# Kernel tuning notes

Hardware: AMD Instinct MI355X
Metric: run time of the kernel (lower is better)

The kernel has to match this reference:

```python
import jax, jax.numpy as jnp
import numpy as np

N = 20000   # nodes
E = 320000  # edges
F0 = 32     # num_features
H = 8       # GAT heads
G = 64      # graphs in batch


def setup_inputs() -> dict:
    key = jax.random.key(0)
    ks = jax.random.split(key, 16)
    def p(k, shape, s=0.05):
        return jax.random.normal(k, shape, jnp.float32) * s
    d = {}
    d['x'] = jax.random.normal(ks[0], (N, F0), jnp.float32)
    d['edge_index'] = jax.random.randint(ks[1], (2, E), 0, N, dtype=jnp.int32)
    d['edge_weights'] = jax.random.uniform(ks[2], (E,), jnp.float32)
    d['batch'] = jnp.sort(jax.random.randint(ks[3], (N,), 0, G, dtype=jnp.int32))
    # GATConv(32 -> 32, heads=8)
    d['W_gat'] = p(ks[4], (F0, H * F0)); d['att_src'] = p(ks[5], (H, F0))
    d['att_dst'] = p(ks[6], (H, F0));    d['b_gat'] = jnp.zeros((H * F0,), jnp.float32)
    # residual Linear(256 -> 1024) (widened so the residual add is shape-consistent)
    d['W_res'] = p(ks[7], (H * F0, 1024)); d['b_res'] = jnp.zeros((1024,), jnp.float32)
    # GCNConv(256 -> 512) + BN1
    d['W2'] = p(ks[8], (H * F0, 512)); d['b2'] = jnp.zeros((512,), jnp.float32)
    d['g1'] = jnp.ones((512,), jnp.float32); d['be1'] = jnp.zeros((512,), jnp.float32)
    d['m1'] = jnp.zeros((512,), jnp.float32); d['v1'] = jnp.ones((512,), jnp.float32)
    # GCNConv(512 -> 1024) + BN2
    d['W3'] = p(ks[9], (512, 1024)); d['b3'] = jnp.zeros((1024,), jnp.float32)
    d['g2'] = jnp.ones((1024,), jnp.float32); d['be2'] = jnp.zeros((1024,), jnp.float32)
    d['m2'] = jnp.zeros((1024,), jnp.float32); d['v2'] = jnp.ones((1024,), jnp.float32)
    # head
    d['Wf1'] = p(ks[10], (1024, 256)); d['bf1'] = jnp.zeros((256,), jnp.float32)
    d['Wf2'] = p(ks[11], (256, 2));    d['bf2'] = jnp.zeros((2,), jnp.float32)
    return d


def _add_self_loops(edge_index, edge_weight, n):
    loop = jnp.arange(n, dtype=edge_index.dtype)
    ei = jnp.concatenate([edge_index, jnp.stack([loop, loop])], axis=1)
    ew = jnp.concatenate([edge_weight, jnp.ones((n,), edge_weight.dtype)])
    return ei, ew


def _gat(x, edge_index, W, att_src, att_dst, b, n):
    # PyG GATConv, concat=True, eval (attention dropout off). Self-loops already added.
    src, dst = edge_index[0], edge_index[1]
    h = (x @ W).reshape(n, H, -1)                    # [N,H,C]
    a_s = jnp.einsum('nhc,hc->nh', h, att_src)        # [N,H]
    a_d = jnp.einsum('nhc,hc->nh', h, att_dst)
    e = jax.nn.leaky_relu(a_s[src] + a_d[dst], 0.2)   # [E,H]
    m = jax.ops.segment_max(e, dst, num_segments=n)   # softmax over incoming edges
    ex = jnp.exp(e - m[dst])
    s = jax.ops.segment_sum(ex, dst, num_segments=n)
    alpha = ex / s[dst]
    out = jax.ops.segment_sum(h[src] * alpha[:, :, None], dst, num_segments=n)
    return out.reshape(n, -1) + b                     # [N,H*C]


def _gcn(x, edge_index, w, W, b, n):
    # PyG GCNConv with symmetric normalization; self-loops (weight 1) already added.
    src, dst = edge_index[0], edge_index[1]
    deg = jax.ops.segment_sum(w, dst, num_segments=n)
    dinv = jnp.where(deg > 0, jax.lax.rsqrt(jnp.maximum(deg, 1e-12)), 0.0)
    norm = dinv[src] * w * dinv[dst]                  # [E]
    h = x @ W                                         # transform first (cheaper)
    return jax.ops.segment_sum(h[src] * norm[:, None], dst, num_segments=n) + b


def _bn(x, g, b, m, v):
    return g * (x - m) * jax.lax.rsqrt(v + 1e-5) + b


def reference(x, edge_index, edge_weights, batch, W_gat, att_src, att_dst, b_gat,
              W_res, b_res, W2, b2, g1, be1, m1, v1, W3, b3, g2, be2, m2, v2,
              Wf1, bf1, Wf2, bf2):
    n = x.shape[0]
    ei, ew = _add_self_loops(edge_index, edge_weights, n)
    h = jax.nn.relu(_gat(x, ei, W_gat, att_src, att_dst, b_gat, n))   # [N,256]
    res = h @ W_res + b_res                                           # [N,1024]
    h = _gcn(h, ei, ew, W2, b2, n)                                    # [N,512]
    h = jax.nn.relu(_bn(h, g1, be1, m1, v1))
    h = _gcn(h, ei, ew, W3, b3, n)                                    # [N,1024]
    h = jax.nn.relu(_bn(h, g2, be2, m2, v2))
    h = h + res
    pooled = jax.ops.segment_max(h, batch, num_segments=G)            # global max pool [G,1024]
    z = jax.nn.relu(pooled @ Wf1 + bf1)                               # dropout is eval no-op
    return z @ Wf2 + bf2                                              # [G,2]
```

## Files before the change

kernel.cpp:

```cpp
#include <hip/hip_runtime.h>
#include <hip/hip_bf16.h>

#define NN 20000
#define EE 320000
#define GG 64
#define EN (EE + NN)
#define MT 157

typedef float f32x4 __attribute__((ext_vector_type(4)));
typedef __bf16 bf16x4 __attribute__((ext_vector_type(4)));
typedef __bf16 bf16x8 __attribute__((ext_vector_type(8)));

__device__ __forceinline__ void gl_lds16(const void* g, void* l) {
    __builtin_amdgcn_global_load_lds((const __attribute__((address_space(1))) void*)g,
                                     (__attribute__((address_space(3))) void*)l, 16, 0, 0);
}

__global__ void sentinel_kernel(float* out, int n) {
    int i = blockIdx.x * 256 + threadIdx.x;
    if (i < n) out[i] = 12345.0f;
}

__global__ void init_kernel(int* deg_cnt, float* deg_w, int* fill, float* pooled) {
    int i = blockIdx.x * 256 + threadIdx.x;
    if (i < NN) { deg_cnt[i] = 1; deg_w[i] = 1.0f; fill[i] = 0; }
    if (i < GG * 1024) pooled[i] = -INFINITY;
}

__global__ __launch_bounds__(256) void convert_wt(const float* __restrict__ W, __bf16* __restrict__ Wt,
                                                  int K, int N) {
    __shared__ float tile[64][65];
    int kb = blockIdx.y * 64, nb = blockIdx.x * 64;
    int tx = threadIdx.x & 63, ty = threadIdx.x >> 6;
#pragma unroll
    for (int i = ty; i < 64; i += 4)
        tile[i][tx] = W[(size_t)(kb + i) * N + nb + tx];
    __syncthreads();
#pragma unroll
    for (int i = ty; i < 64; i += 4)
        Wt[(size_t)(nb + i) * K + kb + tx] = (__bf16)tile[tx][i];
}

__global__ __launch_bounds__(256) void gat_transform(
    const float* __restrict__ x, const float* __restrict__ W,
    const float* __restrict__ att_s, const float* __restrict__ att_d,
    __bf16* __restrict__ hlin, float* __restrict__ a_s, float* __restrict__ a_d)
{
    __shared__ float Ws[32 * 256];
    int tid = threadIdx.x;
#pragma unroll
    for (int k = 0; k < 32; k++) Ws[k * 256 + tid] = W[k * 256 + tid];
    float asc = att_s[tid], adc = att_d[tid];
    __syncthreads();
    for (int n = blockIdx.x; n < NN; n += gridDim.x) {
        const float* xp = x + (size_t)n * 32;
        float acc = 0.f;
#pragma unroll
        for (int k = 0; k < 32; k++) acc += xp[k] * Ws[k * 256 + tid];
        hlin[(size_t)n * 256 + tid] = (__bf16)acc;
        float s = acc * asc, d = acc * adc;
#pragma unroll
        for (int m = 1; m <= 16; m <<= 1) { s += __shfl_xor(s, m); d += __shfl_xor(d, m); }
        if ((tid & 31) == 0) { int h = tid >> 5; a_s[n * 8 + h] = s; a_d[n * 8 + h] = d; }
    }
}

__global__ void deg_kernel(const int* __restrict__ ei, const float* __restrict__ ew,
                           int* deg_cnt, float* deg_w) {
    int e = blockIdx.x * 256 + threadIdx.x;
    if (e >= EE) return;
    int dst = ei[EE + e];
    atomicAdd(&deg_cnt[dst], 1);
    atomicAdd(&deg_w[dst], ew[e]);
}

__global__ __launch_bounds__(256) void scan_kernel(const int* __restrict__ deg_cnt, int* __restrict__ rowptr) {
    __shared__ int partial[256];
    int tid = threadIdx.x;
    const int chunk = (NN + 255) / 256;
    int s0 = tid * chunk, s1 = min(s0 + chunk, NN);
    int sum = 0;
    for (int i = s0; i < s1; i++) sum += deg_cnt[i];
    partial[tid] = sum;
    __syncthreads();
    if (tid == 0) {
        int run = 0;
        for (int i = 0; i < 256; i++) { int t = partial[i]; partial[i] = run; run += t; }
        rowptr[NN] = run;
    }
    __syncthreads();
    int run = partial[tid];
    for (int i = s0; i < s1; i++) { rowptr[i] = run; run += deg_cnt[i]; }
}

__global__ void fill_kernel(const int* __restrict__ ei, const float* __restrict__ ew,
                            const float* __restrict__ deg_w, const int* __restrict__ rowptr,
                            int* fill, int* __restrict__ csr_src, float* __restrict__ csr_norm) {
    int e = blockIdx.x * 256 + threadIdx.x;
    if (e >= EN) return;
    int src, dst; float w;
    if (e < EE) { src = ei[e]; dst = ei[EE + e]; w = ew[e]; }
    else        { src = dst = e - EE; w = 1.0f; }
    int pos = atomicAdd(&fill[dst], 1);
    int slot = rowptr[dst] + pos;
    csr_src[slot] = src;
    csr_norm[slot] = rsqrtf(deg_w[src]) * w * rsqrtf(deg_w[dst]);
}

__global__ __launch_bounds__(256) void gat_agg(
    const int* __restrict__ rowptr, const int* __restrict__ csr_src,
    const float* __restrict__ a_s, const float* __restrict__ a_d,
    const __bf16* __restrict__ hlin, const float* __restrict__ b_gat,
    __bf16* __restrict__ h1)
{
    int widx = threadIdx.x >> 6, lane = threadIdx.x & 63;
    int node = blockIdx.x * 4 + widx;
    int base = rowptr[node], deg = rowptr[node + 1] - base;
    int hA = lane & 7;
    int eslot = lane >> 3;
    int hB = lane >> 3;
    float adA = a_d[node * 8 + hA];
    float acc0[4] = {}, acc1[4] = {}, acc2[4] = {}, acc3[4] = {};

    if (deg <= 64) {
        int sv = (lane < deg) ? csr_src[base + lane] : 0;
        float ev[8];
        float psum = 0.f;
#pragma unroll
        for (int j = 0; j < 8; j++) {
            int e = j * 8 + eslot;
            float v = 0.f;
            if (e < deg) {
                int src = __shfl(sv, e);
                float t = a_s[src * 8 + hA] + adA;
                t = (t > 0.f) ? t : 0.2f * t;
                v = __expf(t);
            }
            ev[j] = v;
            psum += v;
        }
#pragma unroll
        for (int m = 8; m <= 32; m <<= 1) psum += __shfl_xor(psum, m);
        float sinv = 1.f / __shfl(psum, hB);
#pragma unroll
        for (int j = 0; j < 8; j++) {
            if (j * 8 >= deg) break;
            int lim = min(8, deg - j * 8);
            int t = 0;
            for (; t + 3 < lim; t += 4) {
                int sA = __shfl(sv, j * 8 + t),     sB = __shfl(sv, j * 8 + t + 1);
                int sC = __shfl(sv, j * 8 + t + 2), sD = __shfl(sv, j * 8 + t + 3);
                float aA = __shfl(ev[j], (t << 3) | hB) * sinv;
                float aB = __shfl(ev[j], ((t + 1) << 3) | hB) * sinv;
                float aC = __shfl(ev[j], ((t + 2) << 3) | hB) * sinv;
                float aD = __shfl(ev[j], ((t + 3) << 3) | hB) * sinv;
                bf16x4 fA = *(const bf16x4*)(hlin + (size_t)sA * 256 + lane * 4);
                bf16x4 fB = *(const bf16x4*)(hlin + (size_t)sB * 256 + lane * 4);
                bf16x4 fC = *(const bf16x4*)(hlin + (size_t)sC * 256 + lane * 4);
                bf16x4 fD = *(const bf16x4*)(hlin + (size_t)sD * 256 + lane * 4);
#pragma unroll
                for (int c = 0; c < 4; c++) {
                    acc0[c] += aA * (float)fA[c]; acc1[c] += aB * (float)fB[c];
                    acc2[c] += aC * (float)fC[c]; acc3[c] += aD * (float)fD[c];
                }
            }
            for (; t < lim; t++) {
                int src = __shfl(sv, j * 8 + t);
                float alpha = __shfl(ev[j], (t << 3) | hB) * sinv;
                bf16x4 f = *(const bf16x4*)(hlin + (size_t)src * 256 + lane * 4);
#pragma unroll
                for (int c = 0; c < 4; c++) acc0[c] += alpha * (float)f[c];
            }
        }
    } else {
        float sum = 0.f;
        for (int e = 0; e < deg; e++) {
            int src = csr_src[base + e];
            float t = a_s[src * 8 + hA] + adA;
            t = (t > 0.f) ? t : 0.2f * t;
            sum += __expf(t);
        }
        float sinv = 1.f / __shfl(sum, hB);
        float adB = a_d[node * 8 + hB];
        for (int e = 0; e < deg; e++) {
            int src = csr_src[base + e];
            float t = a_s[src * 8 + hB] + adB;
            t = (t > 0.f) ? t : 0.2f * t;
            float alpha = __expf(t) * sinv;
            bf16x4 f = *(const bf16x4*)(hlin + (size_t)src * 256 + lane * 4);
#pragma unroll
            for (int c = 0; c < 4; c++) acc0[c] += alpha * (float)f[c];
        }
    }
    float4 bg = *(const float4*)(b_gat + lane * 4);
    bf16x4 o;
    o[0] = (__bf16)fmaxf(acc0[0] + acc1[0] + acc2[0] + acc3[0] + bg.x, 0.f);
    o[1] = (__bf16)fmaxf(acc0[1] + acc1[1] + acc2[1] + acc3[1] + bg.y, 0.f);
    o[2] = (__bf16)fmaxf(acc0[2] + acc1[2] + acc2[2] + acc3[2] + bg.z, 0.f);
    o[3] = (__bf16)fmaxf(acc0[3] + acc1[3] + acc2[3] + acc3[3] + bg.w, 0.f);
    *(bf16x4*)(h1 + (size_t)node * 256 + lane * 4) = o;
}

template <int C>
__global__ __launch_bounds__(256) void gcn_agg(
    const int* __restrict__ rowptr, const int* __restrict__ csr_src,
    const float* __restrict__ csr_norm, const __bf16* __restrict__ feat,
    __bf16* __restrict__ out)
{
    constexpr int V = C / 64;
    int widx = threadIdx.x >> 6, lane = threadIdx.x & 63;
    int node = blockIdx.x * 4 + widx;
    int base = rowptr[node], deg = rowptr[node + 1] - base;
    float acc0[V], acc1[V], acc2[V], acc3[V];
#pragma unroll
    for (int j = 0; j < V; j++) { acc0[j] = 0.f; acc1[j] = 0.f; acc2[j] = 0.f; acc3[j] = 0.f; }
    const __bf16* fb = feat + lane * V;
    typedef __bf16 bf16v __attribute__((ext_vector_type(V)));
    for (int e0 = 0; e0 < deg; e0 += 64) {
        int cnt = min(64, deg - e0);
        int sv = 0; float wv = 0.f;
        if (lane < cnt) { sv = csr_src[base + e0 + lane]; wv = csr_norm[base + e0 + lane]; }
        int s = 0;
        for (; s + 3 < cnt; s += 4) {
            int sA = __shfl(sv, s),     sB = __shfl(sv, s + 1);
            int sC = __shfl(sv, s + 2), sD = __shfl(sv, s + 3);
            float wA = __shfl(wv, s),     wB = __shfl(wv, s + 1);
            float wC = __shfl(wv, s + 2), wD = __shfl(wv, s + 3);
            bf16v fA = *(const bf16v*)(fb + (size_t)sA * C);
            bf16v fB = *(const bf16v*)(fb + (size_t)sB * C);
            bf16v fC = *(const bf16v*)(fb + (size_t)sC * C);
            bf16v fD = *(const bf16v*)(fb + (size_t)sD * C);
#pragma unroll
            for (int j = 0; j < V; j++) {
                acc0[j] += wA * (float)fA[j]; acc1[j] += wB * (float)fB[j];
                acc2[j] += wC * (float)fC[j]; acc3[j] += wD * (float)fD[j];
            }
        }
        for (; s < cnt; s++) {
            int src = __shfl(sv, s);
            float w = __shfl(wv, s);
            bf16v f = *(const bf16v*)(fb + (size_t)src * C);
#pragma unroll
            for (int j = 0; j < V; j++) acc0[j] += w * (float)f[j];
        }
    }
    bf16v o;
#pragma unroll
    for (int j = 0; j < V; j++) o[j] = (__bf16)(acc0[j] + acc1[j] + acc2[j] + acc3[j]);
    *(bf16v*)(out + (size_t)node * C + lane * V) = o;
}


__device__ __forceinline__ void stage_async(
    const __bf16* __restrict__ A, int K, const __bf16* __restrict__ Wt,
    int bm, int bn, int k0, int tid, __bf16* As, __bf16* Bs)
{
#pragma unroll
    for (int i = 0; i < 2; i++) {
        int j = i * 256 + tid;
        int r = j >> 2, c = j & 3;
        const __bf16* gp = A + (size_t)(bm + r) * K + k0 + c * 8;
        gl_lds16(gp, As + (size_t)(j & ~63) * 8);
    }
#pragma unroll
    for (int i = 0; i < 2; i++) {
        int j = i * 256 + tid;
        int r = j >> 2, c = j & 3;
        const __bf16* gp = Wt + (size_t)(bn + r) * K + k0 + c * 8;
        gl_lds16(gp, Bs + (size_t)(j & ~63) * 8);
    }
}

__device__ __forceinline__ void mfma_step(
    const __bf16* As, const __bf16* Bs, int wr, int wc, int l16, int q, f32x4 (&acc)[4][4])
{
    bf16x8 af[4], bfv[4];
#pragma unroll
    for (int mt = 0; mt < 4; mt++) af[mt]  = *(const bf16x8*)(As + (wr * 64 + mt * 16 + l16) * 32 + q * 8);
#pragma unroll
    for (int nt = 0; nt < 4; nt++) bfv[nt] = *(const bf16x8*)(Bs + (wc * 64 + nt * 16 + l16) * 32 + q * 8);
#pragma unroll
    for (int mt = 0; mt < 4; mt++)
#pragma unroll
        for (int nt = 0; nt < 4; nt++)
            acc[mt][nt] = __builtin_amdgcn_mfma_f32_16x16x32_bf16(af[mt], bfv[nt], acc[mt][nt], 0, 0, 0);
}

__device__ __forceinline__ void gemm_loop(
    const __bf16* __restrict__ A, int K, const __bf16* __restrict__ Wt,
    int bm, int bn, int tid, int wr, int wc, int l16, int q,
    __bf16* As, __bf16* Bs, f32x4 (&acc)[4][4])
{
    for (int k0 = 0; k0 < K; k0 += 32) {
        stage_async(A, K, Wt, bm, bn, k0, tid, As, Bs);
        __syncthreads();
        mfma_step(As, Bs, wr, wc, l16, q, acc);
        __syncthreads();
    }
}

__global__ __launch_bounds__(256) void gemm_bn_relu(
    const __bf16* __restrict__ A, const __bf16* __restrict__ Wt,
    int M, int K, int Nc,
    const float* __restrict__ bias,
    const float* __restrict__ g, const float* __restrict__ be,
    const float* __restrict__ mu, const float* __restrict__ var,
    __bf16* __restrict__ C)
{
    __shared__ __bf16 As[128 * 32];
    __shared__ __bf16 Bs[128 * 32];
    int tid = threadIdx.x;
    int w = tid >> 6, wr = w >> 1, wc = w & 1;
    int l = tid & 63, q = l >> 4, l16 = l & 15;
    int i = blockIdx.x;
    int k = (i & 3) * MT + (i >> 2);
    int bm = (k >> 2) * 128, bn = (k & 3) * 128;
    f32x4 acc[4][4] = {};
    gemm_loop(A, K, Wt, bm, bn, tid, wr, wc, l16, q, As, Bs, acc);
#pragma unroll
    for (int nt = 0; nt < 4; nt++) {
        int gn = bn + wc * 64 + nt * 16 + l16;
        float s = g[gn] * rsqrtf(var[gn] + 1e-5f);
        float t = be[gn] - mu[gn] * s;
        float bv = bias[gn];
#pragma unroll
        for (int mt = 0; mt < 4; mt++)
#pragma unroll
            for (int r = 0; r < 4; r++) {
                int gm = bm + wr * 64 + mt * 16 + q * 4 + r;
                if (gm < M) C[(size_t)gm * Nc + gn] = (__bf16)fmaxf((acc[mt][nt][r] + bv) * s + t, 0.f);
            }
    }
}

__device__ __forceinline__ void atomicMaxFloat(float* addr, float value) {
    if (value >= 0.f) atomicMax((int*)addr, __float_as_int(value));
    else              atomicMin((unsigned int*)addr, __float_as_uint(value));
}

__global__ __launch_bounds__(256) void gemm_final(
    const __bf16* __restrict__ A1, const __bf16* __restrict__ W3t,
    const __bf16* __restrict__ A2, const __bf16* __restrict__ Wrt,
    const float* __restrict__ b3, const float* __restrict__ bres,
    const float* __restrict__ g, const float* __restrict__ be,
    const float* __restrict__ mu, const float* __restrict__ var,
    const int* __restrict__ batch, float* __restrict__ pooled)
{
    const int M = NN;
    __shared__ __bf16 As[128 * 32];
    __shared__ __bf16 Bs[128 * 32];
    __shared__ int bat[128];
    int tid = threadIdx.x;
    int w = tid >> 6, wr = w >> 1, wc = w & 1;
    int l = tid & 63, q = l >> 4, l16 = l & 15;
    int i = blockIdx.x;
    int k = (i & 7) * MT + (i >> 3);
    int bm = (k >> 3) * 128, bn = (k & 7) * 128;
    if (tid < 128) bat[tid] = (bm + tid < M) ? batch[bm + tid] : -1;
    f32x4 acc[4][4] = {};
    f32x4 accR[4][4] = {};
    gemm_loop(A1, 512, W3t, bm, bn, tid, wr, wc, l16, q, As, Bs, acc);
    gemm_loop(A2, 256, Wrt, bm, bn, tid, wr, wc, l16, q, As, Bs, accR);
#pragma unroll
    for (int nt = 0; nt < 4; nt++) {
        int gn = bn + wc * 64 + nt * 16 + l16;
        float s = g[gn] * rsqrtf(var[gn] + 1e-5f);
        float t = be[gn] - mu[gn] * s;
        float bv3 = b3[gn];
        float bvr = bres[gn];
        int cb = -1; float run = 0.f;
#pragma unroll
        for (int mt = 0; mt < 4; mt++)
#pragma unroll
            for (int r = 0; r < 4; r++) {
                int lr = wr * 64 + mt * 16 + q * 4 + r;
                int id = bat[lr];
                if (id < 0) continue;
                float v = fmaxf((acc[mt][nt][r] + bv3) * s + t, 0.f) + accR[mt][nt][r] + bvr;
                if (id == cb) run = fmaxf(run, v);
                else {
                    if (cb >= 0) atomicMaxFloat(&pooled[cb * 1024 + gn], run);
                    cb = id; run = v;
                }
            }
        if (cb >= 0) atomicMaxFloat(&pooled[cb * 1024 + gn], run);
    }
}

__global__ __launch_bounds__(256) void head_kernel(
    const float* __restrict__ pooled, const float* __restrict__ Wf1, const float* __restrict__ bf1,
    const float* __restrict__ Wf2, const float* __restrict__ bf2, float* __restrict__ out)
{
    int gph = blockIdx.x, tid = threadIdx.x;
    __shared__ float prow[1024];
    __shared__ float zred[256];
    for (int i = tid; i < 1024; i += 256) prow[i] = pooled[gph * 1024 + i];
    __syncthreads();
    float z = 0.f;
    for (int k = 0; k < 1024; k++) z += prow[k] * Wf1[k * 256 + tid];
    z = fmaxf(z + bf1[tid], 0.f);
    for (int c = 0; c < 2; c++) {
        zred[tid] = z * Wf2[tid * 2 + c];
        __syncthreads();
        for (int s = 128; s > 0; s >>= 1) { if (tid < s) zred[tid] += zred[tid + s]; __syncthreads(); }
        if (tid == 0) out[gph * 2 + c] = zred[0] + bf2[c];
        __syncthreads();
    }
}

extern "C" void kernel_launch(void* const* d_in, const int* in_sizes, int n_in,
                              void* d_out, int out_size, void* d_ws, size_t ws_size,
                              hipStream_t stream) {
    const float* x       = (const float*)d_in[0];
    const int*   ei      = (const int*)d_in[1];
    const float* ew      = (const float*)d_in[2];
    const int*   batch   = (const int*)d_in[3];
    const float* W_gat   = (const float*)d_in[4];
    const float* att_src = (const float*)d_in[5];
    const float* att_dst = (const float*)d_in[6];
    const float* b_gat   = (const float*)d_in[7];
    const float* W_res   = (const float*)d_in[8];
    const float* b_res   = (const float*)d_in[9];
    const float* W2      = (const float*)d_in[10];
    const float* b2v     = (const float*)d_in[11];
    const float* g1      = (const float*)d_in[12];
    const float* be1     = (const float*)d_in[13];
    const float* m1      = (const float*)d_in[14];
    const float* v1      = (const float*)d_in[15];
    const float* W3      = (const float*)d_in[16];
    const float* b3      = (const float*)d_in[17];
    const float* g2      = (const float*)d_in[18];
    const float* be2     = (const float*)d_in[19];
    const float* m2      = (const float*)d_in[20];
    const float* v2      = (const float*)d_in[21];
    const float* Wf1     = (const float*)d_in[22];
    const float* bf1     = (const float*)d_in[23];
    const float* Wf2     = (const float*)d_in[24];
    const float* bf2v    = (const float*)d_in[25];
    float* out           = (float*)d_out;

    char* ws = (char*)d_ws;
    size_t off = 0;
    auto alloc = [&](size_t bytes) { size_t o = off; off += (bytes + 255) & ~(size_t)255; return o; };
    size_t o_hlin   = alloc((size_t)NN * 256 * 2);
    size_t o_h1     = alloc((size_t)NN * 256 * 2);
    size_t o_h2     = alloc((size_t)NN * 512 * 2);
    size_t o_agg2   = alloc((size_t)NN * 512 * 2);
    size_t o_as     = alloc((size_t)NN * 8 * 4);
    size_t o_ad     = alloc((size_t)NN * 8 * 4);
    size_t o_degc   = alloc((size_t)NN * 4);
    size_t o_degw   = alloc((size_t)NN * 4);
    size_t o_rowptr = alloc((size_t)(NN + 1) * 4);
    size_t o_fill   = alloc((size_t)NN * 4);
    size_t o_csrs   = alloc((size_t)EN * 4);
    size_t o_csrn   = alloc((size_t)EN * 4);
    size_t o_pool   = alloc((size_t)GG * 1024 * 4);
    size_t o_w2t    = alloc((size_t)512 * 256 * 2);
    size_t o_w3t    = alloc((size_t)1024 * 512 * 2);
    size_t o_wrt    = alloc((size_t)1024 * 256 * 2);
    if (off > ws_size) {
        sentinel_kernel<<<(out_size + 255) / 256, 256, 0, stream>>>(out, out_size);
        return;
    }

    __bf16* hlin   = (__bf16*)(ws + o_hlin);
    __bf16* agg1   = hlin;
    __bf16* h1     = (__bf16*)(ws + o_h1);
    __bf16* h2     = (__bf16*)(ws + o_h2);
    __bf16* agg2   = (__bf16*)(ws + o_agg2);
    float*  a_s    = (float*)(ws + o_as);
    float*  a_d    = (float*)(ws + o_ad);
    int*    degc   = (int*)(ws + o_degc);
    float*  degw   = (float*)(ws + o_degw);
    int*    rowptr = (int*)(ws + o_rowptr);
    int*    fillb  = (int*)(ws + o_fill);
    int*    csrs   = (int*)(ws + o_csrs);
    float*  csrn   = (float*)(ws + o_csrn);
    float*  pooled = (float*)(ws + o_pool);
    __bf16* W2t    = (__bf16*)(ws + o_w2t);
    __bf16* W3t    = (__bf16*)(ws + o_w3t);
    __bf16* Wrt    = (__bf16*)(ws + o_wrt);

    init_kernel<<<256, 256, 0, stream>>>(degc, degw, fillb, pooled);
    convert_wt<<<dim3(512 / 64, 256 / 64), 256, 0, stream>>>(W2, W2t, 256, 512);
    convert_wt<<<dim3(1024 / 64, 512 / 64), 256, 0, stream>>>(W3, W3t, 512, 1024);
    convert_wt<<<dim3(1024 / 64, 256 / 64), 256, 0, stream>>>(W_res, Wrt, 256, 1024);

    gat_transform<<<512, 256, 0, stream>>>(x, W_gat, att_src, att_dst, hlin, a_s, a_d);
    deg_kernel<<<(EE + 255) / 256, 256, 0, stream>>>(ei, ew, degc, degw);
    scan_kernel<<<1, 256, 0, stream>>>(degc, rowptr);
    fill_kernel<<<(EN + 255) / 256, 256, 0, stream>>>(ei, ew, degw, rowptr, fillb, csrs, csrn);
    gat_agg<<<NN / 4, 256, 0, stream>>>(rowptr, csrs, a_s, a_d, hlin, b_gat, h1);

    gcn_agg<256><<<NN / 4, 256, 0, stream>>>(rowptr, csrs, csrn, h1, agg1);
    gemm_bn_relu<<<4 * MT, 256, 0, stream>>>(agg1, W2t, NN, 256, 512, b2v,
        g1, be1, m1, v1, h2);
    gcn_agg<512><<<NN / 4, 256, 0, stream>>>(rowptr, csrs, csrn, h2, agg2);
    gemm_final<<<8 * MT, 256, 0, stream>>>(agg2, W3t, h1, Wrt,
        b3, b_res, g2, be2, m2, v2, batch, pooled);

    head_kernel<<<GG, 256, 0, stream>>>(pooled, Wf1, bf1, Wf2, bf2v, out);
}
```

Before: 453.7 us.

## Double GEMM K-tile to 64 with XOR-swizzled LDS and narrow aggregation unroll

The GEMM mainloop now stages a 64-wide K slice per iteration into LDS using an XOR swizzle on the 16-byte column chunks. MFMA fragment reads apply the same swizzle, which halves the number of barrier pairs per K and is meant to avoid LDS bank conflicts. Separately, the GAT and GCN gather loops drop from four independent accumulators to two, reducing register pressure at the cost of fewer loads in flight. The LDS tile size doubles, which may lower occupancy.

```diff
diff --git a/kernel.cpp b/kernel.cpp
--- a/kernel.cpp
+++ b/kernel.cpp
@@ -120,7 +120,8 @@
     int eslot = lane >> 3;
     int hB = lane >> 3;
     float adA = a_d[node * 8 + hA];
-    float acc0[4] = {}, acc1[4] = {}, acc2[4] = {}, acc3[4] = {};
+    float acc0[4] = {0.f, 0.f, 0.f, 0.f};
+    float acc1[4] = {0.f, 0.f, 0.f, 0.f};
 
     if (deg <= 64) {
         int sv = (lane < deg) ? csr_src[base + lane] : 0;
@@ -147,25 +148,19 @@
             if (j * 8 >= deg) break;
             int lim = min(8, deg - j * 8);
             int t = 0;
-            for (; t + 3 < lim; t += 4) {
-                int sA = __shfl(sv, j * 8 + t),     sB = __shfl(sv, j * 8 + t + 1);
-                int sC = __shfl(sv, j * 8 + t + 2), sD = __shfl(sv, j * 8 + t + 3);
+            for (; t + 1 < lim; t += 2) {
+                int s0 = j * 8 + t, s1 = s0 + 1;
+                int srcA = __shfl(sv, s0), srcB = __shfl(sv, s1);
                 float aA = __shfl(ev[j], (t << 3) | hB) * sinv;
                 float aB = __shfl(ev[j], ((t + 1) << 3) | hB) * sinv;
-                float aC = __shfl(ev[j], ((t + 2) << 3) | hB) * sinv;
-                float aD = __shfl(ev[j], ((t + 3) << 3) | hB) * sinv;
-                bf16x4 fA = *(const bf16x4*)(hlin + (size_t)sA * 256 + lane * 4);
-                bf16x4 fB = *(const bf16x4*)(hlin + (size_t)sB * 256 + lane * 4);
-                bf16x4 fC = *(const bf16x4*)(hlin + (size_t)sC * 256 + lane * 4);
-                bf16x4 fD = *(const bf16x4*)(hlin + (size_t)sD * 256 + lane * 4);
-#pragma unroll
-                for (int c = 0; c < 4; c++) {
-                    acc0[c] += aA * (float)fA[c]; acc1[c] += aB * (float)fB[c];
-                    acc2[c] += aC * (float)fC[c]; acc3[c] += aD * (float)fD[c];
-                }
+                bf16x4 fA = *(const bf16x4*)(hlin + (size_t)srcA * 256 + lane * 4);
+                bf16x4 fB = *(const bf16x4*)(hlin + (size_t)srcB * 256 + lane * 4);
+#pragma unroll
+                for (int c = 0; c < 4; c++) { acc0[c] += aA * (float)fA[c]; acc1[c] += aB * (float)fB[c]; }
             }
-            for (; t < lim; t++) {
-                int src = __shfl(sv, j * 8 + t);
+            if (t < lim) {
+                int s0 = j * 8 + t;
+                int src = __shfl(sv, s0);
                 float alpha = __shfl(ev[j], (t << 3) | hB) * sinv;
                 bf16x4 f = *(const bf16x4*)(hlin + (size_t)src * 256 + lane * 4);
 #pragma unroll
@@ -194,10 +189,10 @@
     }
     float4 bg = *(const float4*)(b_gat + lane * 4);
     bf16x4 o;
-    o[0] = (__bf16)fmaxf(acc0[0] + acc1[0] + acc2[0] + acc3[0] + bg.x, 0.f);
-    o[1] = (__bf16)fmaxf(acc0[1] + acc1[1] + acc2[1] + acc3[1] + bg.y, 0.f);
-    o[2] = (__bf16)fmaxf(acc0[2] + acc1[2] + acc2[2] + acc3[2] + bg.z, 0.f);
-    o[3] = (__bf16)fmaxf(acc0[3] + acc1[3] + acc2[3] + acc3[3] + bg.w, 0.f);
+    o[0] = (__bf16)fmaxf(acc0[0] + acc1[0] + bg.x, 0.f);
+    o[1] = (__bf16)fmaxf(acc0[1] + acc1[1] + bg.y, 0.f);
+    o[2] = (__bf16)fmaxf(acc0[2] + acc1[2] + bg.z, 0.f);
+    o[3] = (__bf16)fmaxf(acc0[3] + acc1[3] + bg.w, 0.f);
     *(bf16x4*)(h1 + (size_t)node * 256 + lane * 4) = o;
 }
 
@@ -211,9 +206,9 @@
     int widx = threadIdx.x >> 6, lane = threadIdx.x & 63;
     int node = blockIdx.x * 4 + widx;
     int base = rowptr[node], deg = rowptr[node + 1] - base;
-    float acc0[V], acc1[V], acc2[V], acc3[V];
-#pragma unroll
-    for (int j = 0; j < V; j++) { acc0[j] = 0.f; acc1[j] = 0.f; acc2[j] = 0.f; acc3[j] = 0.f; }
+    float acc0[V], acc1[V];
+#pragma unroll
+    for (int j = 0; j < V; j++) { acc0[j] = 0.f; acc1[j] = 0.f; }
     const __bf16* fb = feat + lane * V;
     typedef __bf16 bf16v __attribute__((ext_vector_type(V)));
     for (int e0 = 0; e0 < deg; e0 += 64) {
@@ -221,22 +216,16 @@
         int sv = 0; float wv = 0.f;
         if (lane < cnt) { sv = csr_src[base + e0 + lane]; wv = csr_norm[base + e0 + lane]; }
         int s = 0;
-        for (; s + 3 < cnt; s += 4) {
-            int sA = __shfl(sv, s),     sB = __shfl(sv, s + 1);
-            int sC = __shfl(sv, s + 2), sD = __shfl(sv, s + 3);
-            float wA = __shfl(wv, s),     wB = __shfl(wv, s + 1);
-            float wC = __shfl(wv, s + 2), wD = __shfl(wv, s + 3);
-            bf16v fA = *(const bf16v*)(fb + (size_t)sA * C);
-            bf16v fB = *(const bf16v*)(fb + (size_t)sB * C);
-            bf16v fC = *(const bf16v*)(fb + (size_t)sC * C);
-            bf16v fD = *(const bf16v*)(fb + (size_t)sD * C);
-#pragma unroll
-            for (int j = 0; j < V; j++) {
-                acc0[j] += wA * (float)fA[j]; acc1[j] += wB * (float)fB[j];
-                acc2[j] += wC * (float)fC[j]; acc3[j] += wD * (float)fD[j];
-            }
-        }
-        for (; s < cnt; s++) {
+#pragma unroll 2
+        for (; s + 1 < cnt; s += 2) {
+            int srcA = __shfl(sv, s),    srcB = __shfl(sv, s + 1);
+            float wA = __shfl(wv, s),    wB   = __shfl(wv, s + 1);
+            bf16v fA = *(const bf16v*)(fb + (size_t)srcA * C);
+            bf16v fB = *(const bf16v*)(fb + (size_t)srcB * C);
+#pragma unroll
+            for (int j = 0; j < V; j++) { acc0[j] += wA * (float)fA[j]; acc1[j] += wB * (float)fB[j]; }
+        }
+        if (s < cnt) {
             int src = __shfl(sv, s);
             float w = __shfl(wv, s);
             bf16v f = *(const bf16v*)(fb + (size_t)src * C);
@@ -246,44 +235,53 @@
     }
     bf16v o;
 #pragma unroll
-    for (int j = 0; j < V; j++) o[j] = (__bf16)(acc0[j] + acc1[j] + acc2[j] + acc3[j]);
+    for (int j = 0; j < V; j++) o[j] = (__bf16)(acc0[j] + acc1[j]);
     *(bf16v*)(out + (size_t)node * C + lane * V) = o;
 }
 
 
-__device__ __forceinline__ void stage_async(
+__device__ __forceinline__ void stage_async64(
     const __bf16* __restrict__ A, int K, const __bf16* __restrict__ Wt,
     int bm, int bn, int k0, int tid, __bf16* As, __bf16* Bs)
 {
 #pragma unroll
-    for (int i = 0; i < 2; i++) {
+    for (int i = 0; i < 4; i++) {
         int j = i * 256 + tid;
-        int r = j >> 2, c = j & 3;
-        const __bf16* gp = A + (size_t)(bm + r) * K + k0 + c * 8;
+        int r = j >> 3, c = j & 7;
+        const __bf16* gp = A + (size_t)(bm + r) * K + k0 + ((c ^ (r & 7)) * 8);
         gl_lds16(gp, As + (size_t)(j & ~63) * 8);
     }
 #pragma unroll
-    for (int i = 0; i < 2; i++) {
+    for (int i = 0; i < 4; i++) {
         int j = i * 256 + tid;
-        int r = j >> 2, c = j & 3;
-        const __bf16* gp = Wt + (size_t)(bn + r) * K + k0 + c * 8;
+        int r = j >> 3, c = j & 7;
+        const __bf16* gp = Wt + (size_t)(bn + r) * K + k0 + ((c ^ (r & 7)) * 8);
         gl_lds16(gp, Bs + (size_t)(j & ~63) * 8);
     }
 }
 
-__device__ __forceinline__ void mfma_step(
+__device__ __forceinline__ void mfma_step64(
     const __bf16* As, const __bf16* Bs, int wr, int wc, int l16, int q, f32x4 (&acc)[4][4])
 {
-    bf16x8 af[4], bfv[4];
-#pragma unroll
-    for (int mt = 0; mt < 4; mt++) af[mt]  = *(const bf16x8*)(As + (wr * 64 + mt * 16 + l16) * 32 + q * 8);
-#pragma unroll
-    for (int nt = 0; nt < 4; nt++) bfv[nt] = *(const bf16x8*)(Bs + (wc * 64 + nt * 16 + l16) * 32 + q * 8);
-#pragma unroll
-    for (int mt = 0; mt < 4; mt++)
-#pragma unroll
-        for (int nt = 0; nt < 4; nt++)
-            acc[mt][nt] = __builtin_amdgcn_mfma_f32_16x16x32_bf16(af[mt], bfv[nt], acc[mt][nt], 0, 0, 0);
+#pragma unroll
+    for (int ks = 0; ks < 2; ks++) {
+        bf16x8 af[4], bfv[4];
+#pragma unroll
+        for (int mt = 0; mt < 4; mt++) {
+            int row = wr * 64 + mt * 16 + l16;
+            af[mt] = *(const bf16x8*)(As + row * 64 + (((ks * 4 + q) ^ (row & 7)) * 8));
+        }
+#pragma unroll
+        for (int nt = 0; nt < 4; nt++) {
+            int row = wc * 64 + nt * 16 + l16;
+            bfv[nt] = *(const bf16x8*)(Bs + row * 64 + (((ks * 4 + q) ^ (row & 7)) * 8));
+        }
+#pragma unroll
+        for (int mt = 0; mt < 4; mt++)
+#pragma unroll
+            for (int nt = 0; nt < 4; nt++)
+                acc[mt][nt] = __builtin_amdgcn_mfma_f32_16x16x32_bf16(af[mt], bfv[nt], acc[mt][nt], 0, 0, 0);
+    }
 }
 
 __device__ __forceinline__ void gemm_loop(
@@ -291,10 +289,10 @@
     int bm, int bn, int tid, int wr, int wc, int l16, int q,
     __bf16* As, __bf16* Bs, f32x4 (&acc)[4][4])
 {
-    for (int k0 = 0; k0 < K; k0 += 32) {
-        stage_async(A, K, Wt, bm, bn, k0, tid, As, Bs);
+    for (int k0 = 0; k0 < K; k0 += 64) {
+        stage_async64(A, K, Wt, bm, bn, k0, tid, As, Bs);
         __syncthreads();
-        mfma_step(As, Bs, wr, wc, l16, q, acc);
+        mfma_step64(As, Bs, wr, wc, l16, q, acc);
         __syncthreads();
     }
 }
@@ -307,8 +305,8 @@
     const float* __restrict__ mu, const float* __restrict__ var,
     __bf16* __restrict__ C)
 {
-    __shared__ __bf16 As[128 * 32];
-    __shared__ __bf16 Bs[128 * 32];
+    __shared__ __bf16 As[128 * 64];
+    __shared__ __bf16 Bs[128 * 64];
     int tid = threadIdx.x;
     int w = tid >> 6, wr = w >> 1, wc = w & 1;
     int l = tid & 63, q = l >> 4, l16 = l & 15;
@@ -347,8 +345,8 @@
     const int* __restrict__ batch, float* __restrict__ pooled)
 {
     const int M = NN;
-    __shared__ __bf16 As[128 * 32];
-    __shared__ __bf16 Bs[128 * 32];
+    __shared__ __bf16 As[128 * 64];
+    __shared__ __bf16 Bs[128 * 64];
     __shared__ int bat[128];
     int tid = threadIdx.x;
     int w = tid >> 6, wr = w >> 1, wc = w & 1;
```

Result: no change. 449.4 us (-1.0%).
